# Kernel optimization log

Measured on AMD Instinct MI355X. Metric: run time of the kernel, lower is better.

Reference implementation:

```python
import jax, jax.numpy as jnp
import numpy as np

B, S, D = 4, 2048, 1024
H = 16
HD = D // H

def setup_inputs() -> dict:
    key = jax.random.key(0)
    ks = jax.random.split(key, 6)
    s = 0.02
    return {
        "input_tensor": jax.random.normal(ks[0], (B, S, D), dtype=jnp.float32),
        "Wq": jax.random.normal(ks[1], (D, D), dtype=jnp.float32) * s,
        "Wk": jax.random.normal(ks[2], (D, D), dtype=jnp.float32) * s,
        "Wv": jax.random.normal(ks[3], (D, D), dtype=jnp.float32) * s,
        "Wo": jax.random.normal(ks[4], (D, D), dtype=jnp.float32) * s,
        "bo": jax.random.normal(ks[5], (D,), dtype=jnp.float32) * s,
    }

def reference(input_tensor, Wq, Wk, Wv, Wo, bo):
    b, n, _ = input_tensor.shape
    # projections (nn.Linear: x @ W.T; bias=False for qkv)
    q = jnp.einsum('bnd,ed->bne', input_tensor, Wq).reshape(b, n, H, HD).transpose(0, 2, 1, 3)
    k = jnp.einsum('bnd,ed->bne', input_tensor, Wk).reshape(b, n, H, HD).transpose(0, 2, 1, 3)
    v = jnp.einsum('bnd,ed->bne', input_tensor, Wv).reshape(b, n, H, HD).transpose(0, 2, 1, 3)
    scores = jnp.einsum('bhqd,bhkd->bhqk', q, k)  # [B,H,S,S]
    causal = jnp.triu(jnp.ones((n, n), dtype=bool), k=1)
    scores = jnp.where(causal, -jnp.inf, scores)
    weights = jax.nn.softmax(scores / jnp.sqrt(jnp.float32(HD)), axis=-1)
    ctx = jnp.einsum('bhqk,bhkd->bhqd', weights, v)  # [B,H,S,HD]
    ctx = ctx.transpose(0, 2, 1, 3).reshape(b, n, D)
    return jnp.einsum('bnd,ed->bne', ctx, Wo) + bo
```

## Files before the change

### kernel.cpp

```cpp
#include <hip/hip_runtime.h>
#include <stdint.h>

#define S_LEN 2048
#define DIM   1024
#define NH    16
#define HD    64
#define BATCH 4
#define M_ROWS (BATCH * S_LEN)
#define PSTR  136

typedef __attribute__((ext_vector_type(8))) __bf16 bf16x8;
typedef __attribute__((ext_vector_type(4))) float  f32x4;

union Frag { bf16x8 v; uint4 q; };

__device__ __forceinline__ ushort f2bf(float f) {
  union { float f; unsigned u; } x; x.f = f;
  unsigned r = x.u + 0x7fffu + ((x.u >> 16) & 1u);
  return (ushort)(r >> 16);
}
__device__ __forceinline__ ushort f2bf_n(float f) {
  union { __bf16 b; ushort u; } x; x.b = (__bf16)f; return x.u;
}

__device__ __forceinline__ f32x4 mfma16(const Frag& a, const Frag& b, f32x4 c) {
  return __builtin_amdgcn_mfma_f32_16x16x32_bf16(a.v, b.v, c, 0, 0, 0);
}

__device__ __forceinline__ void gld_lds16(const ushort* g, ushort* l) {
  __builtin_amdgcn_global_load_lds(
      (__attribute__((address_space(1))) void*)g,
      (__attribute__((address_space(3))) void*)l, 16, 0, 0);
}

__global__ void cast_x_kernel(const float* __restrict__ src, ushort* __restrict__ dst) {
  int i = blockIdx.x * 256 + threadIdx.x;
  float4 f = ((const float4*)src)[i];
  ushort4 u; u.x = f2bf(f.x); u.y = f2bf(f.y); u.z = f2bf(f.z); u.w = f2bf(f.w);
  ((ushort4*)dst)[i] = u;
}

__global__ void cast_w_kernel(const float* __restrict__ w0, const float* __restrict__ w1,
                              const float* __restrict__ w2, const float* __restrict__ w3,
                              ushort* __restrict__ d0, ushort* __restrict__ d1,
                              ushort* __restrict__ d2, ushort* __restrict__ d3) {
  const float* s; ushort* d;
  int z = blockIdx.y;
  if (z == 0) { s = w0; d = d0; } else if (z == 1) { s = w1; d = d1; }
  else if (z == 2) { s = w2; d = d2; } else { s = w3; d = d3; }
  int i = blockIdx.x * 256 + threadIdx.x;
  float4 f = ((const float4*)s)[i];
  ushort4 u; u.x = f2bf(f.x); u.y = f2bf(f.y); u.z = f2bf(f.z); u.w = f2bf(f.w);
  ((ushort4*)d)[i] = u;
}

template <int MODE>
__global__ __launch_bounds__(256)
void gemm_bk64(const ushort* __restrict__ A,
               const ushort* __restrict__ B0, const ushort* __restrict__ B1,
               const ushort* __restrict__ B2,
               ushort* __restrict__ Qb, ushort* __restrict__ Kb, ushort* __restrict__ Vtb,
               float* __restrict__ outf, const float* __restrict__ bias, float scaleq) {
  __shared__ __align__(16) ushort As[128 * 64];
  __shared__ __align__(16) ushort Bs[128 * 64];
  const int K = DIM;
  int lane = threadIdx.x & 63, wave = threadIdx.x >> 6;
  int quad = lane >> 4, l15 = lane & 15;

  const int GX = (MODE == 0) ? 24 : 8;
  int lin = blockIdx.x + GX * blockIdx.y;
  int xcd = lin & 7, idx = lin >> 3;
  int by = xcd * 8 + idx / GX;
  int bx = idx % GX;

  int rowBase = by * 128;
  int wsel, colBase;
  const ushort* Bt;
  if (MODE == 0) {
    wsel = bx >> 3;
    colBase = (bx & 7) * 128;
    Bt = (wsel == 0) ? B0 : (wsel == 1) ? B1 : B2;
  } else {
    wsel = 0;
    colBase = bx * 128;
    Bt = B0;
  }
  int wm = (wave >> 1) * 64, wn = (wave & 1) * 64;
  bool swapT = (MODE == 1) || (wsel < 2);

  const ushort* Ag = A + (size_t)rowBase * K;
  const ushort* Bg = Bt + (size_t)colBase * K;

  f32x4 acc[4][4];
#pragma unroll
  for (int i = 0; i < 4; i++)
#pragma unroll
    for (int j = 0; j < 4; j++) acc[i][j] = (f32x4){0.f, 0.f, 0.f, 0.f};

  for (int k0 = 0; k0 < K; k0 += 64) {
#pragma unroll
    for (int cc = 0; cc < 4; ++cc) {
      int c = wave * 4 + cc;
      int s = c * 64 + lane;
      int row = s >> 3;
      int c8 = (s & 7) ^ (row & 7);
      gld_lds16(Ag + (size_t)row * K + k0 + c8 * 8, &As[c * 512]);
      gld_lds16(Bg + (size_t)row * K + k0 + c8 * 8, &Bs[c * 512]);
    }
    __syncthreads();
    Frag af[4][2], bf[4][2];
#pragma unroll
    for (int t = 0; t < 4; t++) {
      int ar = wm + t * 16 + l15;
      int br = wn + t * 16 + l15;
#pragma unroll
      for (int kk = 0; kk < 2; kk++) {
        af[t][kk].q = *(const uint4*)&As[ar * 64 + (((kk * 4 + quad) ^ (ar & 7))) * 8];
        bf[t][kk].q = *(const uint4*)&Bs[br * 64 + (((kk * 4 + quad) ^ (br & 7))) * 8];
      }
    }
    if (swapT) {
#pragma unroll
      for (int kk = 0; kk < 2; kk++)
#pragma unroll
        for (int i = 0; i < 4; i++)
#pragma unroll
          for (int j = 0; j < 4; j++) acc[i][j] = mfma16(bf[j][kk], af[i][kk], acc[i][j]);
    } else {
#pragma unroll
      for (int kk = 0; kk < 2; kk++)
#pragma unroll
        for (int i = 0; i < 4; i++)
#pragma unroll
          for (int j = 0; j < 4; j++) acc[i][j] = mfma16(af[i][kk], bf[j][kk], acc[i][j]);
    }
    __syncthreads();
  }

  if (MODE == 0 && wsel == 2) {
#pragma unroll
    for (int i = 0; i < 4; i++) {
      int rowt = wm + i * 16 + quad * 4;
#pragma unroll
      for (int j = 0; j < 4; j++) {
        int e = colBase + wn + j * 16 + l15;
        int h = e >> 6, hd = e & 63;
        int m0 = rowBase + rowt;
        int b = m0 >> 11, s0 = m0 & (S_LEN - 1);
        ushort4 u;
        u.x = f2bf(acc[i][j][0]); u.y = f2bf(acc[i][j][1]);
        u.z = f2bf(acc[i][j][2]); u.w = f2bf(acc[i][j][3]);
        *(ushort4*)&Vtb[((size_t)((b * NH + h) * HD + hd) << 11) + s0] = u;
      }
    }
  } else if (MODE == 0) {
    ushort* dst = wsel ? Kb : Qb;
    float sc = wsel ? 1.f : scaleq;
#pragma unroll
    for (int i = 0; i < 4; i++) {
      size_t m = (size_t)(rowBase + wm + i * 16 + l15);
#pragma unroll
      for (int j = 0; j < 4; j++) {
        int e = colBase + wn + j * 16 + quad * 4;
        ushort4 u;
        u.x = f2bf(acc[i][j][0] * sc); u.y = f2bf(acc[i][j][1] * sc);
        u.z = f2bf(acc[i][j][2] * sc); u.w = f2bf(acc[i][j][3] * sc);
        *(ushort4*)&dst[m * DIM + e] = u;
      }
    }
  } else {
#pragma unroll
    for (int i = 0; i < 4; i++) {
      size_t m = (size_t)(rowBase + wm + i * 16 + l15);
#pragma unroll
      for (int j = 0; j < 4; j++) {
        int e = colBase + wn + j * 16 + quad * 4;
        float4 bv = *(const float4*)&bias[e];
        float4 o;
        o.x = acc[i][j][0] + bv.x; o.y = acc[i][j][1] + bv.y;
        o.z = acc[i][j][2] + bv.z; o.w = acc[i][j][3] + bv.w;
        *(float4*)&outf[m * DIM + e] = o;
      }
    }
  }
}

__global__ __launch_bounds__(256)
void flash_attn(const ushort* __restrict__ Qb, const ushort* __restrict__ Kb,
                const ushort* __restrict__ Vtb, ushort* __restrict__ Ctx) {
  __shared__ __align__(16) ushort Ks[128 * 64];
  __shared__ __align__(16) ushort Vs[64 * 128];
  __shared__ __align__(16) ushort Ps[4][16 * PSTR];

  int lane = threadIdx.x & 63, wave = threadIdx.x >> 6;
  int quad = lane >> 4, l15 = lane & 15;
  int bh = blockIdx.x;
  int wq0 = wave * 32;
  int b = bh >> 4, h = bh & 15;

  const ushort* Qg = Qb + (size_t)b * S_LEN * DIM + h * HD;
  const ushort* Kg = Kb + (size_t)b * S_LEN * DIM + h * HD;
  const ushort* Vh = Vtb + (size_t)bh * HD * S_LEN;
  ushort* Pw = Ps[wave];

  const int NQT = S_LEN / 128;

#pragma unroll 1
  for (int pass = 0; pass < 2; ++pass) {
    int qt = pass ? blockIdx.y : (NQT - 1 - blockIdx.y);
    int q0 = qt * 128;

#pragma unroll
    for (int cc = 0; cc < 4; ++cc) {
      int c = wave * 4 + cc;
      int s = c * 64 + lane;
      int row = s >> 3;
      int c8 = (s & 7) ^ (row & 7);
      gld_lds16(Qg + (size_t)(q0 + row) * DIM + c8 * 8, &Ks[c * 512]);
    }
    __syncthreads();
    Frag qf[2][2];
#pragma unroll
    for (int it = 0; it < 2; ++it)
#pragma unroll
      for (int ks = 0; ks < 2; ++ks) {
        int row = wq0 + it * 16 + l15;
        int c8 = (ks * 4 + quad) ^ (row & 7);
        qf[it][ks].q = *(const uint4*)&Ks[row * 64 + c8 * 8];
      }
    __syncthreads();

    float lst[2] = {0.f, 0.f};
    f32x4 oacc[2][4];
#pragma unroll
    for (int it = 0; it < 2; ++it)
#pragma unroll
      for (int dt = 0; dt < 4; ++dt) oacc[it][dt] = (f32x4){0.f, 0.f, 0.f, 0.f};

#pragma unroll 1
    for (int kt = 0; kt <= qt; ++kt) {
#pragma unroll
      for (int cc = 0; cc < 4; ++cc) {
        int c = wave * 4 + cc;
        int s = c * 64 + lane;
        int krow = s >> 3;
        int kc8 = (s & 7) ^ (krow & 7);
        gld_lds16(Kg + (size_t)(kt * 128 + krow) * DIM + kc8 * 8, &Ks[c * 512]);
        int vrow = s >> 4;
        int vc8 = (s & 15) ^ (vrow & 15);
        gld_lds16(Vh + (size_t)vrow * S_LEN + kt * 128 + vc8 * 8, &Vs[c * 512]);
      }
      __syncthreads();

      f32x4 sacc[2][8];
#pragma unroll
      for (int jt = 0; jt < 8; ++jt) {
        int row = jt * 16 + l15;
        Frag kf0, kf1;
        kf0.q = *(const uint4*)&Ks[row * 64 + ((quad) ^ (row & 7)) * 8];
        kf1.q = *(const uint4*)&Ks[row * 64 + ((4 + quad) ^ (row & 7)) * 8];
#pragma unroll
        for (int it = 0; it < 2; ++it) {
          f32x4 a = (f32x4){0.f, 0.f, 0.f, 0.f};
          a = mfma16(kf0, qf[it][0], a);
          a = mfma16(kf1, qf[it][1], a);
          sacc[it][jt] = a;
        }
      }

      if (kt == qt) {
#pragma unroll
        for (int it = 0; it < 2; ++it)
#pragma unroll
          for (int jt = 0; jt < 8; ++jt)
#pragma unroll
            for (int r = 0; r < 4; ++r)
              if (jt * 16 + quad * 4 + r > wq0 + it * 16 + l15)
                sacc[it][jt][r] = -1e30f;
      }

#pragma unroll
      for (int it = 0; it < 2; ++it) {
        float ps = 0.f;
#pragma unroll
        for (int jt = 0; jt < 8; ++jt) {
          float p0 = exp2f(sacc[it][jt][0]);
          float p1 = exp2f(sacc[it][jt][1]);
          float p2 = exp2f(sacc[it][jt][2]);
          float p3 = exp2f(sacc[it][jt][3]);
          ps += (p0 + p1) + (p2 + p3);
          ushort4 u; u.x = f2bf_n(p0); u.y = f2bf_n(p1); u.z = f2bf_n(p2); u.w = f2bf_n(p3);
          *(ushort4*)&Pw[l15 * PSTR + jt * 16 + quad * 4] = u;
        }
        ps += __shfl_xor(ps, 16);
        ps += __shfl_xor(ps, 32);
        lst[it] += ps;

        Frag pf[4];
#pragma unroll
        for (int ks = 0; ks < 4; ++ks)
          pf[ks].q = *(const uint4*)&Pw[l15 * PSTR + ks * 32 + quad * 8];

#pragma unroll
        for (int dt = 0; dt < 4; ++dt) {
          f32x4 a = oacc[it][dt];
#pragma unroll
          for (int ks = 0; ks < 4; ++ks) {
            int row = dt * 16 + l15;
            Frag vf;
            vf.q = *(const uint4*)&Vs[row * 128 + (((ks * 4 + quad) ^ (row & 15))) * 8];
            a = mfma16(pf[ks], vf, a);
          }
          oacc[it][dt] = a;
        }
      }
      __syncthreads();
    }

#pragma unroll
    for (int it = 0; it < 2; ++it) {
      float linv = 1.f / lst[it];
      float lr[4];
#pragma unroll
      for (int r = 0; r < 4; ++r) lr[r] = __shfl(linv, quad * 4 + r);
#pragma unroll
      for (int r = 0; r < 4; ++r) {
        int qg = q0 + wq0 + it * 16 + quad * 4 + r;
        size_t base = ((size_t)(b * S_LEN + qg)) * DIM + h * HD;
#pragma unroll
        for (int dt = 0; dt < 4; ++dt)
          Ctx[base + dt * 16 + l15] = f2bf_n(oacc[it][dt][r] * lr[r]);
      }
    }
    __syncthreads();
  }
}

extern "C" void kernel_launch(void* const* d_in, const int* in_sizes, int n_in,
                              void* d_out, int out_size, void* d_ws, size_t ws_size,
                              hipStream_t stream) {
  (void)in_sizes; (void)n_in; (void)out_size; (void)ws_size;
  const float* x  = (const float*)d_in[0];
  const float* Wq = (const float*)d_in[1];
  const float* Wk = (const float*)d_in[2];
  const float* Wv = (const float*)d_in[3];
  const float* Wo = (const float*)d_in[4];
  const float* bo = (const float*)d_in[5];
  float* out = (float*)d_out;

  ushort* Xb  = (ushort*)d_ws;
  ushort* Wqb = Xb  + (size_t)M_ROWS * DIM;
  ushort* Wkb = Wqb + (size_t)DIM * DIM;
  ushort* Wvb = Wkb + (size_t)DIM * DIM;
  ushort* Wob = Wvb + (size_t)DIM * DIM;
  ushort* Qb  = Wob + (size_t)DIM * DIM;
  ushort* Kb  = Qb  + (size_t)M_ROWS * DIM;
  ushort* Vtb = Kb  + (size_t)M_ROWS * DIM;
  ushort* Ctx = Vtb + (size_t)M_ROWS * DIM;

  const float SCALE_Q = 0.18033688011112042f;

  cast_x_kernel<<<dim3(M_ROWS * DIM / 1024), 256, 0, stream>>>(x, Xb);
  cast_w_kernel<<<dim3(DIM * DIM / 1024, 4), 256, 0, stream>>>(Wq, Wk, Wv, Wo, Wqb, Wkb, Wvb, Wob);

  gemm_bk64<0><<<dim3(24, 64), 256, 0, stream>>>(Xb, Wqb, Wkb, Wvb, Qb, Kb, Vtb,
                                                 nullptr, nullptr, SCALE_Q);

  flash_attn<<<dim3(BATCH * NH, S_LEN / 256), 256, 0, stream>>>(Qb, Kb, Vtb, Ctx);

  gemm_bk64<1><<<dim3(8, 64), 256, 0, stream>>>(Ctx, Wob, nullptr, nullptr, nullptr, nullptr,
                                                nullptr, out, bo, 1.0f);
}
```

Before: 276.1 us.

## Register-prefetch next K tile in GEMM and attention instead of direct LDS loads

Replaces the direct global-to-LDS async loads in both the projection GEMM and the flash-attention K/V loop with a register-staged software pipeline. The next tile is loaded into registers right after the barrier, so its latency overlaps the current tile's MFMA work, then stored to LDS at the top of the next iteration. The swizzled global offsets are precomputed once outside the loop. This costs extra VGPRs (16 uint4 per thread) and explicit LDS stores, which may lower occupancy. The single LDS buffer still needs a barrier before each overwrite.

```diff
diff --git a/kernel.cpp b/kernel.cpp
--- a/kernel.cpp
+++ b/kernel.cpp
@@ -91,23 +91,42 @@
   const ushort* Ag = A + (size_t)rowBase * K;
   const ushort* Bg = Bt + (size_t)colBase * K;
 
+  size_t goff[4];
+#pragma unroll
+  for (int cc = 0; cc < 4; ++cc) {
+    int c = wave * 4 + cc, s = c * 64 + lane;
+    int row = s >> 3, c8 = (s & 7) ^ (row & 7);
+    goff[cc] = (size_t)row * K + c8 * 8;
+  }
+
   f32x4 acc[4][4];
 #pragma unroll
   for (int i = 0; i < 4; i++)
 #pragma unroll
     for (int j = 0; j < 4; j++) acc[i][j] = (f32x4){0.f, 0.f, 0.f, 0.f};
+
+  uint4 pa[4], pb[4];
+#pragma unroll
+  for (int cc = 0; cc < 4; ++cc) {
+    pa[cc] = *(const uint4*)(Ag + goff[cc]);
+    pb[cc] = *(const uint4*)(Bg + goff[cc]);
+  }
 
   for (int k0 = 0; k0 < K; k0 += 64) {
 #pragma unroll
     for (int cc = 0; cc < 4; ++cc) {
       int c = wave * 4 + cc;
-      int s = c * 64 + lane;
-      int row = s >> 3;
-      int c8 = (s & 7) ^ (row & 7);
-      gld_lds16(Ag + (size_t)row * K + k0 + c8 * 8, &As[c * 512]);
-      gld_lds16(Bg + (size_t)row * K + k0 + c8 * 8, &Bs[c * 512]);
+      *(uint4*)&As[c * 512 + lane * 8] = pa[cc];
+      *(uint4*)&Bs[c * 512 + lane * 8] = pb[cc];
     }
     __syncthreads();
+    if (k0 + 64 < K) {
+#pragma unroll
+      for (int cc = 0; cc < 4; ++cc) {
+        pa[cc] = *(const uint4*)(Ag + goff[cc] + (k0 + 64));
+        pb[cc] = *(const uint4*)(Bg + goff[cc] + (k0 + 64));
+      }
+    }
     Frag af[4][2], bf[4][2];
 #pragma unroll
     for (int t = 0; t < 4; t++) {
@@ -203,6 +222,25 @@
   const ushort* Vh = Vtb + (size_t)bh * HD * S_LEN;
   ushort* Pw = Ps[wave];
 
+  size_t koff[4], voff[4];
+#pragma unroll
+  for (int cc = 0; cc < 4; ++cc) {
+    int c = wave * 4 + cc, s = c * 64 + lane;
+    int krow = s >> 3, kc8 = (s & 7) ^ (krow & 7);
+    koff[cc] = (size_t)krow * DIM + kc8 * 8;
+    int vrow = s >> 4, vc8 = (s & 15) ^ (vrow & 15);
+    voff[cc] = (size_t)vrow * S_LEN + vc8 * 8;
+  }
+
+  uint4 pk[4], pv[4];
+  auto load_kv = [&](int kt) {
+#pragma unroll
+    for (int cc = 0; cc < 4; ++cc) {
+      pk[cc] = *(const uint4*)(Kg + koff[cc] + (size_t)kt * 128 * DIM);
+      pv[cc] = *(const uint4*)(Vh + voff[cc] + kt * 128);
+    }
+  };
+
   const int NQT = S_LEN / 128;
 
 #pragma unroll 1
@@ -218,6 +256,7 @@
       int c8 = (s & 7) ^ (row & 7);
       gld_lds16(Qg + (size_t)(q0 + row) * DIM + c8 * 8, &Ks[c * 512]);
     }
+    load_kv(0);
     __syncthreads();
     Frag qf[2][2];
 #pragma unroll
@@ -242,15 +281,11 @@
 #pragma unroll
       for (int cc = 0; cc < 4; ++cc) {
         int c = wave * 4 + cc;
-        int s = c * 64 + lane;
-        int krow = s >> 3;
-        int kc8 = (s & 7) ^ (krow & 7);
-        gld_lds16(Kg + (size_t)(kt * 128 + krow) * DIM + kc8 * 8, &Ks[c * 512]);
-        int vrow = s >> 4;
-        int vc8 = (s & 15) ^ (vrow & 15);
-        gld_lds16(Vh + (size_t)vrow * S_LEN + kt * 128 + vc8 * 8, &Vs[c * 512]);
+        *(uint4*)&Ks[c * 512 + lane * 8] = pk[cc];
+        *(uint4*)&Vs[c * 512 + lane * 8] = pv[cc];
       }
       __syncthreads();
+      if (kt < qt) load_kv(kt + 1);
 
       f32x4 sacc[2][8];
 #pragma unroll
```

Measured after the change: 506.1 us. 1.83x slower.
